# Kernel tuning notes

Measured on AMD Instinct MI355X. Metric: run time of the kernel, lower is better.

Reference implementation:

```python
import jax, jax.numpy as jnp
import numpy as np

D_MODEL, D_STATE, EXPAND = 1024, 128, 2
E = D_MODEL * EXPAND          # 2048
N = D_STATE                   # 128
H = 1
P = E
TD = D_STATE // 2             # 64
Z_DIM = E + E + N + N + H + H + TD + H  # 4369
EPS = 1e-05
B_SZ, L = 4, 2048


def setup_inputs() -> dict:
    key = jax.random.key(0)
    ks = jax.random.split(key, 6)
    u = jax.random.normal(ks[0], (B_SZ, L, D_MODEL), dtype=jnp.float32)
    W_in = jax.random.normal(ks[1], (Z_DIM, D_MODEL), dtype=jnp.float32) * 0.02
    W_out = jax.random.normal(ks[2], (D_MODEL, E), dtype=jnp.float32) * 0.02
    w_normB = jnp.ones((N,), jnp.float32)
    w_normC = jnp.ones((N,), jnp.float32)
    B_bias = jnp.ones((N,), jnp.float32)
    C_bias = jnp.ones((N,), jnp.float32)
    # dt_bias buffer: dt_i ~ logU(0.001, 0.1); dt_bias = dt_i + log(-expm1(-dt_i))
    dt_i = jnp.exp(jax.random.uniform(ks[3], (H,)) * (np.log(0.1) - np.log(0.001)) + np.log(0.001))
    dt_i = jnp.clip(dt_i, 1e-4, None)
    dt_bias = dt_i + jnp.log(-jnp.expm1(-dt_i))
    A_log = jnp.full((H,), np.log(0.5), jnp.float32)
    return {"u": u, "W_in": W_in, "w_normB": w_normB, "w_normC": w_normC,
            "B_bias": B_bias, "C_bias": C_bias, "dt_bias": dt_bias,
            "A_log": A_log, "W_out": W_out}


def _rms(x, w):
    return x * jax.lax.rsqrt(jnp.mean(x * x, axis=-1, keepdims=True) + EPS) * w


def _rope(x, ang):
    half = x.shape[-1] // 2
    x1, x2 = x[..., :half], x[..., half:]
    c, s = jnp.cos(ang), jnp.sin(ang)
    return jnp.concatenate([x1 * c - x2 * s, x1 * s + x2 * c], axis=-1)


def reference(u, W_in, w_normB, w_normC, B_bias, C_bias, dt_bias, A_log, W_out):
    Bb, Ls, _ = u.shape
    z = u @ W_in.T  # [B, L, Z_DIM]
    o = 0
    def take(n):
        nonlocal o
        r = z[..., o:o + n]; o += n; return r
    x = jax.nn.silu(take(E))
    gate = jax.nn.silu(take(E))
    B_ = take(N)
    C_ = take(N)
    dt_ = take(H)
    A_ = take(H)
    th = take(TD)
    lam_ = take(H)

    dt = jax.nn.softplus(dt_ + dt_bias)          # [B, L, H]
    A = -jax.nn.softplus(A_ + A_log)             # [B, L, H]
    lam = jax.nn.sigmoid(lam_)                   # [B, L, H]
    alpha = jnp.exp(dt * A)                      # [B, L, H]

    B_ = _rms(B_, w_normB) + B_bias
    C_ = _rms(C_, w_normC) + C_bias
    ca = jnp.cumsum(jnp.mean(dt, axis=-1, keepdims=True) * th, axis=1)  # [B, L, TD]
    B_ = _rope(B_, ca)
    C_ = _rope(C_, ca)

    xh = x.reshape(Bb, Ls, H, P)
    xp = jnp.concatenate([jnp.zeros_like(xh[:, :1]), xh[:, :-1]], axis=1)  # roll + zero t=0
    lh = lam[..., None]
    xt = lh * xh + (1.0 - lh) * alpha[..., None] * xp  # [B, L, H, P]

    # fallback SSM: per-channel mean drive, per-head scalar A (mean over batch+time)
    u_mean = jnp.mean(xt, axis=-1)               # [B, L, H]
    A_bar = jnp.mean(A, axis=(0, 1))             # [H]
    dA = jnp.exp(dt * A_bar)                     # [B, L, H]
    dBu = dt[..., None] * B_[:, :, None, :] * u_mean[..., None]  # [B, L, H, N]

    def step(state, xs):
        dA_t, dBu_t, C_t = xs                    # [B,H], [B,H,N], [B,N]
        state = dA_t[..., None] * state + dBu_t  # [B, H, N]
        y_t = jnp.einsum('bhn,bn->bh', state, C_t)
        return state, y_t

    state0 = jnp.zeros((Bb, H, N), dtype=xt.dtype)
    _, ys = jax.lax.scan(step, state0,
                         (jnp.moveaxis(dA, 1, 0), jnp.moveaxis(dBu, 1, 0), jnp.moveaxis(C_, 1, 0)))
    outs = jnp.moveaxis(ys, 0, 1)                # [B, L, H]
    y = jnp.broadcast_to(outs, (Bb, Ls, E))      # H=1 expanded to E
    return (y * gate) @ W_out.T
```

## Files before the change

### kernel.cpp

```cpp
#include <hip/hip_runtime.h>
#include <cstdint>
#include <cstddef>

typedef __bf16 bf16_t;
typedef bf16_t bf16x8 __attribute__((ext_vector_type(8)));
typedef float f32x4 __attribute__((ext_vector_type(4)));

#define B_SZ    4
#define LSEQ    2048
#define DMODEL  1024
#define EDIM    2048
#define NSTATE  128
#define ZDIM    4419
#define ZPAD    4608
#define ROWS    (B_SZ*LSEQ)
#define EPSV    1e-5f

#define SCHUNK  128
#define SCLEN   (LSEQ/SCHUNK)
#define RCH     128
#define RCLEN   (LSEQ/RCH)

__device__ __forceinline__ float softplus_f(float x){
  return fmaxf(x, 0.f) + log1pf(expf(-fabsf(x)));
}
__device__ __forceinline__ float sigmoid_f(float x){ return 1.f/(1.f+expf(-x)); }
__device__ __forceinline__ float silu_f(float x){ return x/(1.f+expf(-x)); }

__device__ __forceinline__ void gload_lds16(const void* g, void* l){
  __builtin_amdgcn_global_load_lds(
      (const __attribute__((address_space(1))) void*)g,
      (__attribute__((address_space(3))) void*)l, 16, 0, 0);
}

__device__ __forceinline__ float blockReduce256(float v, float* red, int t){
  red[t] = v; __syncthreads();
  #pragma unroll
  for (int off = 128; off > 0; off >>= 1){
    if (t < off) red[t] += red[t+off];
    __syncthreads();
  }
  float r = red[0];
  __syncthreads();
  return r;
}

__global__ __launch_bounds__(256) void prep_kernel(
    const float* __restrict__ u, const float* __restrict__ win, const float* __restrict__ wout,
    bf16_t* __restrict__ ubf, bf16_t* __restrict__ winbf, bf16_t* __restrict__ woutbf,
    float* __restrict__ Asum)
{
  size_t i = (size_t)blockIdx.x*256 + threadIdx.x;
  if (i == 0) Asum[0] = 0.f;
  const size_t NU = (size_t)ROWS*DMODEL;
  const size_t NW = (size_t)ZPAD*DMODEL;
  const size_t NO = (size_t)DMODEL*EDIM;
  if (i < NU){ ubf[i] = (bf16_t)u[i]; return; }
  i -= NU;
  if (i < NW){
    size_t n = i >> 10;
    winbf[i] = (n < (size_t)ZDIM) ? (bf16_t)win[i] : (bf16_t)0.f;
    return;
  }
  i -= NW;
  if (i < NO) woutbf[i] = (bf16_t)wout[i];
}

template<int BM, int KDIM, int MODE>
__global__ __launch_bounds__(512, 2) void gemm8_kernel(
    const bf16_t* __restrict__ A, const bf16_t* __restrict__ W,
    bf16_t* __restrict__ o_x, bf16_t* __restrict__ o_g, float* __restrict__ o_z,
    const float* __restrict__ scale, float* __restrict__ o_f)
{
  constexpr int BN  = 256;
  constexpr int NT  = KDIM/64;
  constexpr int MR  = BM/32;
  constexpr int BUFE = (BM+BN)*64;
  __shared__ __align__(16) bf16_t lds[BUFE*2];

  const int tid  = threadIdx.x;
  const int wid  = tid>>6, lane = tid&63;
  const int wr   = wid>>2, wc = wid&3;
  const int m0   = blockIdx.y*BM, n0 = blockIdx.x*BN;
  const int lr   = lane&15;

  f32x4 acc[MR][4] = {};

  auto stage = [&](int buf, int t){
    bf16_t* lA = lds + buf*BUFE;
    bf16_t* lB = lA + BM*64;
    const int k0 = t*64;
    #pragma unroll
    for (int q = 0; q < BM/64; ++q){
      int cidx = q*512 + tid;
      int row = cidx>>3, sc = (cidx&7) ^ (row&7);
      gload_lds16(A + (size_t)(m0+row)*KDIM + k0 + sc*8,
                  lA + (size_t)(q*512 + wid*64)*8);
    }
    #pragma unroll
    for (int q = 0; q < BN/64; ++q){
      int cidx = q*512 + tid;
      int row = cidx>>3, sc = (cidx&7) ^ (row&7);
      gload_lds16(W + (size_t)(n0+row)*KDIM + k0 + sc*8,
                  lB + (size_t)(q*512 + wid*64)*8);
    }
  };

  stage(0, 0);
  __syncthreads();
  int cur = 0;
  for (int t = 0; t < NT; ++t){
    if (t+1 < NT) stage(cur^1, t+1);
    const bf16_t* lA = lds + cur*BUFE;
    const bf16_t* lB = lA + BM*64;
    #pragma unroll
    for (int kk = 0; kk < 2; ++kk){
      const int g = kk*4 + (lane>>4);
      bf16x8 bfr[4], af[MR];
      #pragma unroll
      for (int n = 0; n < 4; ++n){
        int rr = wc*64 + n*16 + lr;
        bfr[n] = *(const bf16x8*)&lB[rr*64 + ((g^(rr&7))<<3)];
      }
      #pragma unroll
      for (int m = 0; m < MR; ++m){
        int rr = wr*(BM/2) + m*16 + lr;
        af[m] = *(const bf16x8*)&lA[rr*64 + ((g^(rr&7))<<3)];
      }
      __builtin_amdgcn_s_setprio(1);
      #pragma unroll
      for (int m = 0; m < MR; ++m)
        #pragma unroll
        for (int n = 0; n < 4; ++n)
          acc[m][n] = __builtin_amdgcn_mfma_f32_16x16x32_bf16(af[m], bfr[n], acc[m][n], 0,0,0);
      __builtin_amdgcn_s_setprio(0);
    }
    __syncthreads();
    cur ^= 1;
  }

  #pragma unroll
  for (int m = 0; m < MR; ++m){
    int rowb = m0 + wr*(BM/2) + m*16 + ((lane>>4)<<2);
    #pragma unroll
    for (int n = 0; n < 4; ++n){
      int col = n0 + wc*64 + n*16 + lr;
      #pragma unroll
      for (int i = 0; i < 4; ++i){
        int r = rowb + i;
        float v = acc[m][n][i];
        if (MODE == 0){
          if (col < 2048)       o_x[(size_t)r*EDIM + col]        = (bf16_t)silu_f(v);
          else if (col < 4096)  o_g[(size_t)r*EDIM + (col-2048)] = (bf16_t)silu_f(v);
          else if (col < 4480)  o_z[(size_t)r*384 + (col-4096)]  = v;
        } else {
          o_f[(size_t)r*DMODEL + col] = v * scale[r];
        }
      }
    }
  }
}

__global__ __launch_bounds__(256) void fuse_kernel(
    const bf16_t* __restrict__ xbuf, const float* __restrict__ zs,
    const float* __restrict__ wnB, const float* __restrict__ wnC,
    const float* __restrict__ Bb, const float* __restrict__ Cb,
    const float* __restrict__ dtb, const float* __restrict__ Alog,
    float* __restrict__ Bn, float* __restrict__ Cn, float* __restrict__ dtth,
    float* __restrict__ dts, float* __restrict__ alphas, float* __restrict__ lams,
    float* __restrict__ xbar, float* Asum)
{
  __shared__ float red[256];
  int r = blockIdx.x, t = threadIdx.x;

  const bf16_t* xr = xbuf + (size_t)r*EDIM;
  bf16x8 xv = *(const bf16x8*)(xr + t*8);
  float s = 0.f;
  #pragma unroll
  for (int i=0;i<8;++i) s += (float)xv[i];
  float xs = blockReduce256(s, red, t);

  const float* zr = zs + (size_t)r*384;
  float dt  = softplus_f(zr[256] + dtb[0]);
  float Av  = -softplus_f(zr[257] + Alog[0]);
  float lam = sigmoid_f(zr[322]);
  float alpha = expf(dt*Av);

  if (t == 0){
    xbar[r]   = xs * (1.f/2048.f);
    dts[r]    = dt;
    alphas[r] = alpha;
    lams[r]   = lam;
    atomicAdd(Asum, Av);
  }
  if (t < 64) dtth[(size_t)r*64 + t] = dt * zr[258+t];

  float bv = (t < 128) ? zr[t]       : 0.f;
  float cv = (t < 128) ? zr[128+t]   : 0.f;
  float b2 = blockReduce256(bv*bv, red, t);
  float c2 = blockReduce256(cv*cv, red, t);
  if (t < 128){
    float rb = rsqrtf(b2*(1.f/128.f) + EPSV);
    float rc = rsqrtf(c2*(1.f/128.f) + EPSV);
    Bn[(size_t)r*128 + t] = bv*rb*wnB[t] + Bb[t];
    Cn[(size_t)r*128 + t] = cv*rc*wnC[t] + Cb[t];
  }
}

__global__ __launch_bounds__(64) void rope_sum_kernel(
    const float* __restrict__ dtth, float* __restrict__ csum)
{
  int b  = blockIdx.x >> 7;
  int ch = blockIdx.x & 127;
  int d  = threadIdx.x;
  const float* base = dtth + ((size_t)b*LSEQ + (size_t)ch*RCLEN)*64 + d;
  float s = 0.f;
  #pragma unroll
  for (int i = 0; i < RCLEN; ++i) s += base[(size_t)i*64];
  csum[((size_t)b*RCH + ch)*64 + d] = s;
}

__global__ __launch_bounds__(64) void rope_prefix_kernel(float* __restrict__ csum)
{
  int b = blockIdx.x, d = threadIdx.x;
  float s = 0.f;
  for (int c = 0; c < RCH; ++c){
    size_t idx = ((size_t)b*RCH + c)*64 + d;
    float v = csum[idx]; csum[idx] = s; s += v;
  }
}

__global__ __launch_bounds__(64) void rope_apply_kernel(
    const float* __restrict__ dtth, const float* __restrict__ csum,
    float* __restrict__ Bn, float* __restrict__ Cn)
{
  int b  = blockIdx.x >> 7;
  int ch = blockIdx.x & 127;
  int d  = threadIdx.x;
  float ca = csum[((size_t)b*RCH + ch)*64 + d];
  int l0 = ch*RCLEN;
  const float* base = dtth + ((size_t)b*LSEQ)*64 + d;
  for (int l = l0; l < l0 + RCLEN; ++l){
    ca += base[(size_t)l*64];
    float sn, cs;
    sincosf(ca, &sn, &cs);
    size_t ro = ((size_t)b*LSEQ + l)*128;
    float b1 = Bn[ro+d], b2v = Bn[ro+64+d];
    Bn[ro+d]    = b1*cs - b2v*sn;
    Bn[ro+64+d] = b1*sn + b2v*cs;
    float c1 = Cn[ro+d], c2v = Cn[ro+64+d];
    Cn[ro+d]    = c1*cs - c2v*sn;
    Cn[ro+64+d] = c1*sn + c2v*cs;
  }
}

__global__ __launch_bounds__(64) void scan_local_kernel(
    const float* __restrict__ dts, const float* __restrict__ alphas,
    const float* __restrict__ lams, const float* __restrict__ xbar,
    const float* __restrict__ Asum,
    const float* __restrict__ Bn, const float* __restrict__ Cn,
    float* __restrict__ ylocal, float* __restrict__ Pfix,
    float* __restrict__ Sfin, float* __restrict__ Dch)
{
  int b  = blockIdx.x / SCHUNK;
  int ch = blockIdx.x % SCHUNK;
  int n  = threadIdx.x;
  float Abar = Asum[0] * (1.f/(float)ROWS);
  float s1 = 0.f, s2 = 0.f, P = 1.f;
  int l0 = ch*SCLEN;
  #pragma unroll
  for (int i = 0; i < SCLEN; ++i){
    int l = l0 + i;
    size_t r = (size_t)b*LSEQ + l;
    float dt = dts[r], lam = lams[r], al = alphas[r], xb = xbar[r];
    float xp = (l > 0) ? xbar[r-1] : 0.f;
    float um = lam*xb + (1.f-lam)*al*xp;
    float dA = expf(dt*Abar);
    float coef = dt*um;
    size_t ro = r*128;
    s1 = dA*s1 + coef*Bn[ro+n];
    s2 = dA*s2 + coef*Bn[ro+64+n];
    P *= dA;
    float p = s1*Cn[ro+n] + s2*Cn[ro+64+n];
    #pragma unroll
    for (int off = 32; off > 0; off >>= 1) p += __shfl_down(p, off);
    if (n == 0){ ylocal[r] = p; Pfix[r] = P; }
  }
  size_t so = ((size_t)b*SCHUNK + ch)*128;
  Sfin[so + n]      = s1;
  Sfin[so + 64 + n] = s2;
  if (n == 0) Dch[b*SCHUNK + ch] = P;
}

__global__ __launch_bounds__(128) void scan_carry_kernel(
    const float* __restrict__ Sfin, const float* __restrict__ Dch,
    float* __restrict__ Sin)
{
  int b = blockIdx.x;
  int n = threadIdx.x;
  float s = 0.f;
  for (int c = 0; c < SCHUNK; ++c){
    size_t so = ((size_t)b*SCHUNK + c)*128;
    Sin[so + n] = s;
    s = Dch[b*SCHUNK + c]*s + Sfin[so + n];
  }
}

__global__ __launch_bounds__(256) void scan_fix_kernel(
    const float* __restrict__ Cn, const float* __restrict__ Sin,
    const float* __restrict__ ylocal, const float* __restrict__ Pfix,
    float* __restrict__ outsv)
{
  int r = blockIdx.x*4 + (threadIdx.x>>6);
  int n = threadIdx.x & 63;
  int b  = r / LSEQ;
  int ch = (r % LSEQ) / SCLEN;
  const float* si = Sin + ((size_t)b*SCHUNK + ch)*128;
  size_t ro = (size_t)r*128;
  float p = Cn[ro+n]*si[n] + Cn[ro+64+n]*si[64+n];
  #pragma unroll
  for (int off = 32; off > 0; off >>= 1) p += __shfl_down(p, off);
  if (n == 0) outsv[r] = ylocal[r] + Pfix[r]*p;
}

extern "C" void kernel_launch(void* const* d_in, const int* in_sizes, int n_in,
                              void* d_out, int out_size, void* d_ws, size_t ws_size,
                              hipStream_t stream)
{
  const float* u    = (const float*)d_in[0];
  const float* W_in = (const float*)d_in[1];
  const float* wnB  = (const float*)d_in[2];
  const float* wnC  = (const float*)d_in[3];
  const float* Bb   = (const float*)d_in[4];
  const float* Cb   = (const float*)d_in[5];
  const float* dtb  = (const float*)d_in[6];
  const float* Alog = (const float*)d_in[7];
  const float* Wout = (const float*)d_in[8];
  float* out = (float*)d_out;
  char* ws = (char*)d_ws;

  constexpr size_t OFF_ASUM = 0;
  constexpr size_t OFF_UBF  = 256;
  constexpr size_t SZ_UBF   = (size_t)ROWS*DMODEL*2;
  constexpr size_t OFF_WIN  = OFF_UBF + SZ_UBF;
  constexpr size_t SZ_WIN   = (size_t)ZPAD*DMODEL*2;
  constexpr size_t OFF_WOUT = OFF_WIN + SZ_WIN;
  constexpr size_t SZ_WOUT  = (size_t)DMODEL*EDIM*2;
  constexpr size_t OFF_X    = OFF_WOUT + SZ_WOUT;
  constexpr size_t SZ_X     = (size_t)ROWS*EDIM*2;
  constexpr size_t OFF_G    = OFF_X + SZ_X;
  constexpr size_t OFF_ZS   = OFF_G + SZ_X;
  constexpr size_t SZ_ZS    = (size_t)ROWS*384*4;
  constexpr size_t OFF_BN   = OFF_ZS + SZ_ZS;
  constexpr size_t SZ_BN    = (size_t)ROWS*128*4;
  constexpr size_t OFF_CN   = OFF_BN + SZ_BN;
  constexpr size_t OFF_DTTH = OFF_CN + SZ_BN;
  constexpr size_t SZ_DTTH  = (size_t)ROWS*64*4;
  constexpr size_t OFF_DT   = OFF_DTTH + SZ_DTTH;
  constexpr size_t OFF_AL   = OFF_DT  + (size_t)ROWS*4;
  constexpr size_t OFF_LAM  = OFF_AL  + (size_t)ROWS*4;
  constexpr size_t OFF_XB   = OFF_LAM + (size_t)ROWS*4;
  constexpr size_t OFF_OUTS = OFF_XB  + (size_t)ROWS*4;
  constexpr size_t OFF_YLOC = OFF_OUTS + (size_t)ROWS*4;
  constexpr size_t OFF_PFIX = OFF_YLOC + (size_t)ROWS*4;
  constexpr size_t OFF_SFIN = OFF_PFIX + (size_t)ROWS*4;
  constexpr size_t SZ_SFIN  = (size_t)B_SZ*SCHUNK*128*4;
  constexpr size_t OFF_DCH  = OFF_SFIN + SZ_SFIN;
  constexpr size_t OFF_SIN  = OFF_DCH + (size_t)B_SZ*SCHUNK*4;
  constexpr size_t OFF_CSUM = OFF_SIN + SZ_SFIN;

  float*  Asum   = (float*) (ws + OFF_ASUM);
  bf16_t* ubf    = (bf16_t*)(ws + OFF_UBF);
  bf16_t* winbf  = (bf16_t*)(ws + OFF_WIN);
  bf16_t* woutbf = (bf16_t*)(ws + OFF_WOUT);
  bf16_t* xbuf   = (bf16_t*)(ws + OFF_X);
  bf16_t* gbuf   = (bf16_t*)(ws + OFF_G);
  float*  zsb    = (float*) (ws + OFF_ZS);
  float*  Bn     = (float*) (ws + OFF_BN);
  float*  Cn     = (float*) (ws + OFF_CN);
  float*  dtth   = (float*) (ws + OFF_DTTH);
  float*  dts    = (float*) (ws + OFF_DT);
  float*  alphas = (float*) (ws + OFF_AL);
  float*  lams   = (float*) (ws + OFF_LAM);
  float*  xbar   = (float*) (ws + OFF_XB);
  float*  outsv  = (float*) (ws + OFF_OUTS);
  float*  ylocal = (float*) (ws + OFF_YLOC);
  float*  Pfix   = (float*) (ws + OFF_PFIX);
  float*  Sfin   = (float*) (ws + OFF_SFIN);
  float*  Dch    = (float*) (ws + OFF_DCH);
  float*  Sin    = (float*) (ws + OFF_SIN);
  float*  csum   = (float*) (ws + OFF_CSUM);

  {
    size_t total = (size_t)ROWS*DMODEL + (size_t)ZPAD*DMODEL + (size_t)DMODEL*EDIM;
    int blocks = (int)((total + 255)/256);
    prep_kernel<<<blocks, 256, 0, stream>>>(u, W_in, Wout, ubf, winbf, woutbf, Asum);
  }
  {
    dim3 g(ZPAD/256, ROWS/256);
    gemm8_kernel<256, DMODEL, 0><<<g, 512, 0, stream>>>(
        ubf, winbf, xbuf, gbuf, zsb, nullptr, nullptr);
  }
  fuse_kernel<<<ROWS, 256, 0, stream>>>(xbuf, zsb, wnB, wnC, Bb, Cb, dtb, Alog,
                                        Bn, Cn, dtth, dts, alphas, lams, xbar, Asum);
  rope_sum_kernel<<<B_SZ*RCH, 64, 0, stream>>>(dtth, csum);
  rope_prefix_kernel<<<B_SZ, 64, 0, stream>>>(csum);
  rope_apply_kernel<<<B_SZ*RCH, 64, 0, stream>>>(dtth, csum, Bn, Cn);
  scan_local_kernel<<<B_SZ*SCHUNK, 64, 0, stream>>>(dts, alphas, lams, xbar, Asum,
                                                    Bn, Cn, ylocal, Pfix, Sfin, Dch);
  scan_carry_kernel<<<B_SZ, 128, 0, stream>>>(Sfin, Dch, Sin);
  scan_fix_kernel<<<ROWS/4, 256, 0, stream>>>(Cn, Sin, ylocal, Pfix, outsv);
  {
    dim3 g(DMODEL/256, ROWS/128);
    gemm8_kernel<128, EDIM, 1><<<g, 512, 0, stream>>>(
        gbuf, woutbf, nullptr, nullptr, nullptr, outsv, out);
  }
}
```

Before: 344.5 us.

## Fuse x row-mean into GEMM epilogue and triple-buffer GEMM pipeline

The first GEMM no longer writes the silu(x) activations to memory. It reduces them per row in the epilogue and adds the partial sums to an fp32 buffer with atomics, which removes a large bf16 store and its reload in fuse_kernel. The GEMM moves to a 3-stage LDS pipeline with explicit vmcnt waits and raw barriers, a 1D grid with XCD-aware block remapping, and BM=128 for the first GEMM. fuse_kernel shrinks to 128 threads. The cost is atomic contention, a non-deterministic summation order, and larger LDS use that may reduce occupancy.

```diff
diff --git a/kernel.cpp b/kernel.cpp
--- a/kernel.cpp
+++ b/kernel.cpp
@@ -10,7 +10,6 @@
 #define LSEQ    2048
 #define DMODEL  1024
 #define EDIM    2048
-#define NSTATE  128
 #define ZDIM    4419
 #define ZPAD    4608
 #define ROWS    (B_SZ*LSEQ)
@@ -33,10 +32,10 @@
       (__attribute__((address_space(3))) void*)l, 16, 0, 0);
 }
 
-__device__ __forceinline__ float blockReduce256(float v, float* red, int t){
+__device__ __forceinline__ float blockReduce128(float v, float* red, int t){
   red[t] = v; __syncthreads();
   #pragma unroll
-  for (int off = 128; off > 0; off >>= 1){
+  for (int off = 64; off > 0; off >>= 1){
     if (t < off) red[t] += red[t+off];
     __syncthreads();
   }
@@ -48,10 +47,11 @@
 __global__ __launch_bounds__(256) void prep_kernel(
     const float* __restrict__ u, const float* __restrict__ win, const float* __restrict__ wout,
     bf16_t* __restrict__ ubf, bf16_t* __restrict__ winbf, bf16_t* __restrict__ woutbf,
-    float* __restrict__ Asum)
+    float* __restrict__ Asum, float* __restrict__ xraw)
 {
   size_t i = (size_t)blockIdx.x*256 + threadIdx.x;
   if (i == 0) Asum[0] = 0.f;
+  if (i < ROWS) xraw[i] = 0.f;
   const size_t NU = (size_t)ROWS*DMODEL;
   const size_t NW = (size_t)ZPAD*DMODEL;
   const size_t NO = (size_t)DMODEL*EDIM;
@@ -66,23 +66,28 @@
   if (i < NO) woutbf[i] = (bf16_t)wout[i];
 }
 
-template<int BM, int KDIM, int MODE>
-__global__ __launch_bounds__(512, 2) void gemm8_kernel(
+template<int BM, int KDIM, int NXT, int MODE>
+__global__ __launch_bounds__(512, 2) void gemmDP_kernel(
     const bf16_t* __restrict__ A, const bf16_t* __restrict__ W,
-    bf16_t* __restrict__ o_x, bf16_t* __restrict__ o_g, float* __restrict__ o_z,
+    float* __restrict__ xraw, bf16_t* __restrict__ o_g, float* __restrict__ o_z,
     const float* __restrict__ scale, float* __restrict__ o_f)
 {
-  constexpr int BN  = 256;
-  constexpr int NT  = KDIM/64;
-  constexpr int MR  = BM/32;
+  constexpr int BN = 256;
+  constexpr int NT = KDIM/64;
+  constexpr int MR = BM/32;
   constexpr int BUFE = (BM+BN)*64;
-  __shared__ __align__(16) bf16_t lds[BUFE*2];
-
-  const int tid  = threadIdx.x;
-  const int wid  = tid>>6, lane = tid&63;
-  const int wr   = wid>>2, wc = wid&3;
-  const int m0   = blockIdx.y*BM, n0 = blockIdx.x*BN;
-  const int lr   = lane&15;
+  __shared__ __align__(16) bf16_t lds[BUFE*3];
+
+  const int tid = threadIdx.x;
+  const int wid = tid>>6, lane = tid&63;
+  const int wr = wid>>2, wc = wid&3;
+  const int lr = lane&15;
+
+  const int nwg = NXT*(ROWS/BM);
+  const int id = blockIdx.x;
+  const int rid = (id & 7)*(nwg>>3) + (id>>3);
+  const int bx = rid % NXT, by = rid / NXT;
+  const int m0 = by*BM, n0 = bx*BN;
 
   f32x4 acc[MR][4] = {};
 
@@ -106,12 +111,8 @@
     }
   };
 
-  stage(0, 0);
-  __syncthreads();
-  int cur = 0;
-  for (int t = 0; t < NT; ++t){
-    if (t+1 < NT) stage(cur^1, t+1);
-    const bf16_t* lA = lds + cur*BUFE;
+  auto compute = [&](int buf){
+    const bf16_t* lA = lds + buf*BUFE;
     const bf16_t* lB = lA + BM*64;
     #pragma unroll
     for (int kk = 0; kk < 2; ++kk){
@@ -135,34 +136,70 @@
           acc[m][n] = __builtin_amdgcn_mfma_f32_16x16x32_bf16(af[m], bfr[n], acc[m][n], 0,0,0);
       __builtin_amdgcn_s_setprio(0);
     }
-    __syncthreads();
-    cur ^= 1;
-  }
-
-  #pragma unroll
-  for (int m = 0; m < MR; ++m){
-    int rowb = m0 + wr*(BM/2) + m*16 + ((lane>>4)<<2);
-    #pragma unroll
-    for (int n = 0; n < 4; ++n){
-      int col = n0 + wc*64 + n*16 + lr;
+  };
+
+  stage(0, 0);
+  stage(1, 1);
+  int cur = 0;
+  for (int t = 0; t + 2 < NT; ++t){
+    int nb = cur + 2; if (nb >= 3) nb -= 3;
+    stage(nb, t+2);
+    asm volatile("s_waitcnt vmcnt(12)" ::: "memory");
+    asm volatile("s_barrier" ::: "memory");
+    compute(cur);
+    asm volatile("s_barrier" ::: "memory");
+    if (++cur == 3) cur = 0;
+  }
+  asm volatile("s_waitcnt vmcnt(6)" ::: "memory");
+  asm volatile("s_barrier" ::: "memory");
+  compute(cur);
+  asm volatile("s_barrier" ::: "memory");
+  if (++cur == 3) cur = 0;
+  asm volatile("s_waitcnt vmcnt(0)" ::: "memory");
+  asm volatile("s_barrier" ::: "memory");
+  compute(cur);
+
+  if (MODE == 0 && n0 < 2048){
+    #pragma unroll
+    for (int m = 0; m < MR; ++m){
       #pragma unroll
       for (int i = 0; i < 4; ++i){
-        int r = rowb + i;
-        float v = acc[m][n][i];
-        if (MODE == 0){
-          if (col < 2048)       o_x[(size_t)r*EDIM + col]        = (bf16_t)silu_f(v);
-          else if (col < 4096)  o_g[(size_t)r*EDIM + (col-2048)] = (bf16_t)silu_f(v);
-          else if (col < 4480)  o_z[(size_t)r*384 + (col-4096)]  = v;
-        } else {
-          o_f[(size_t)r*DMODEL + col] = v * scale[r];
+        float p = 0.f;
+        #pragma unroll
+        for (int n = 0; n < 4; ++n) p += silu_f(acc[m][n][i]);
+        #pragma unroll
+        for (int off = 8; off > 0; off >>= 1) p += __shfl_xor(p, off);
+        if (lr == 0){
+          int r = m0 + wr*(BM/2) + m*16 + ((lane>>4)<<2) + i;
+          atomicAdd(xraw + r, p);
         }
       }
     }
-  }
-}
-
-__global__ __launch_bounds__(256) void fuse_kernel(
-    const bf16_t* __restrict__ xbuf, const float* __restrict__ zs,
+  } else {
+    #pragma unroll
+    for (int m = 0; m < MR; ++m){
+      int rowb = m0 + wr*(BM/2) + m*16 + ((lane>>4)<<2);
+      #pragma unroll
+      for (int n = 0; n < 4; ++n){
+        int col = n0 + wc*64 + n*16 + lr;
+        #pragma unroll
+        for (int i = 0; i < 4; ++i){
+          int r = rowb + i;
+          float v = acc[m][n][i];
+          if (MODE == 0){
+            if (col < 4096)      o_g[(size_t)r*EDIM + (col-2048)] = (bf16_t)silu_f(v);
+            else if (col < 4480) o_z[(size_t)r*384 + (col-4096)]  = v;
+          } else {
+            o_f[(size_t)r*DMODEL + col] = v * scale[r];
+          }
+        }
+      }
+    }
+  }
+}
+
+__global__ __launch_bounds__(128) void fuse_kernel(
+    const float* __restrict__ xraw, const float* __restrict__ zs,
     const float* __restrict__ wnB, const float* __restrict__ wnC,
     const float* __restrict__ Bb, const float* __restrict__ Cb,
     const float* __restrict__ dtb, const float* __restrict__ Alog,
@@ -170,40 +207,27 @@
     float* __restrict__ dts, float* __restrict__ alphas, float* __restrict__ lams,
     float* __restrict__ xbar, float* Asum)
 {
-  __shared__ float red[256];
+  __shared__ float red[128];
   int r = blockIdx.x, t = threadIdx.x;
-
-  const bf16_t* xr = xbuf + (size_t)r*EDIM;
-  bf16x8 xv = *(const bf16x8*)(xr + t*8);
-  float s = 0.f;
-  #pragma unroll
-  for (int i=0;i<8;++i) s += (float)xv[i];
-  float xs = blockReduce256(s, red, t);
-
   const float* zr = zs + (size_t)r*384;
-  float dt  = softplus_f(zr[256] + dtb[0]);
-  float Av  = -softplus_f(zr[257] + Alog[0]);
-  float lam = sigmoid_f(zr[322]);
-  float alpha = expf(dt*Av);
-
+  float bv = zr[t], cv = zr[128+t];
+  float b2 = blockReduce128(bv*bv, red, t);
+  float c2 = blockReduce128(cv*cv, red, t);
+  float rb = rsqrtf(b2*(1.f/128.f) + EPSV);
+  float rc = rsqrtf(c2*(1.f/128.f) + EPSV);
+  Bn[(size_t)r*128 + t] = bv*rb*wnB[t] + Bb[t];
+  Cn[(size_t)r*128 + t] = cv*rc*wnC[t] + Cb[t];
+
+  float dt = softplus_f(zr[256] + dtb[0]);
+  if (t < 64) dtth[(size_t)r*64 + t] = dt * zr[258+t];
   if (t == 0){
-    xbar[r]   = xs * (1.f/2048.f);
+    float Av  = -softplus_f(zr[257] + Alog[0]);
+    float lam = sigmoid_f(zr[322]);
     dts[r]    = dt;
-    alphas[r] = alpha;
+    alphas[r] = expf(dt*Av);
     lams[r]   = lam;
+    xbar[r]   = xraw[r] * (1.f/2048.f);
     atomicAdd(Asum, Av);
-  }
-  if (t < 64) dtth[(size_t)r*64 + t] = dt * zr[258+t];
-
-  float bv = (t < 128) ? zr[t]       : 0.f;
-  float cv = (t < 128) ? zr[128+t]   : 0.f;
-  float b2 = blockReduce256(bv*bv, red, t);
-  float c2 = blockReduce256(cv*cv, red, t);
-  if (t < 128){
-    float rb = rsqrtf(b2*(1.f/128.f) + EPSV);
-    float rc = rsqrtf(c2*(1.f/128.f) + EPSV);
-    Bn[(size_t)r*128 + t] = bv*rb*wnB[t] + Bb[t];
-    Cn[(size_t)r*128 + t] = cv*rc*wnC[t] + Cb[t];
   }
 }
 
@@ -373,7 +397,7 @@
   bf16_t* ubf    = (bf16_t*)(ws + OFF_UBF);
   bf16_t* winbf  = (bf16_t*)(ws + OFF_WIN);
   bf16_t* woutbf = (bf16_t*)(ws + OFF_WOUT);
-  bf16_t* xbuf   = (bf16_t*)(ws + OFF_X);
+  float*  xraw   = (float*) (ws + OFF_X);
   bf16_t* gbuf   = (bf16_t*)(ws + OFF_G);
   float*  zsb    = (float*) (ws + OFF_ZS);
   float*  Bn     = (float*) (ws + OFF_BN);
@@ -394,14 +418,11 @@
   {
     size_t total = (size_t)ROWS*DMODEL + (size_t)ZPAD*DMODEL + (size_t)DMODEL*EDIM;
     int blocks = (int)((total + 255)/256);
-    prep_kernel<<<blocks, 256, 0, stream>>>(u, W_in, Wout, ubf, winbf, woutbf, Asum);
-  }
-  {
-    dim3 g(ZPAD/256, ROWS/256);
-    gemm8_kernel<256, DMODEL, 0><<<g, 512, 0, stream>>>(
-        ubf, winbf, xbuf, gbuf, zsb, nullptr, nullptr);
-  }
-  fuse_kernel<<<ROWS, 256, 0, stream>>>(xbuf, zsb, wnB, wnC, Bb, Cb, dtb, Alog,
+    prep_kernel<<<blocks, 256, 0, stream>>>(u, W_in, Wout, ubf, winbf, woutbf, Asum, xraw);
+  }
+  gemmDP_kernel<128, DMODEL, ZPAD/256, 0><<<(ZPAD/256)*(ROWS/128), 512, 0, stream>>>(
+      ubf, winbf, xraw, gbuf, zsb, nullptr, nullptr);
+  fuse_kernel<<<ROWS, 128, 0, stream>>>(xraw, zsb, wnB, wnC, Bb, Cb, dtb, Alog,
                                         Bn, Cn, dtth, dts, alphas, lams, xbar, Asum);
   rope_sum_kernel<<<B_SZ*RCH, 64, 0, stream>>>(dtth, csum);
   rope_prefix_kernel<<<B_SZ, 64, 0, stream>>>(csum);
@@ -410,9 +431,6 @@
                                                     Bn, Cn, ylocal, Pfix, Sfin, Dch);
   scan_carry_kernel<<<B_SZ, 128, 0, stream>>>(Sfin, Dch, Sin);
   scan_fix_kernel<<<ROWS/4, 256, 0, stream>>>(Cn, Sin, ylocal, Pfix, outsv);
-  {
-    dim3 g(DMODEL/256, ROWS/128);
-    gemm8_kernel<128, EDIM, 1><<<g, 512, 0, stream>>>(
-        gbuf, woutbf, nullptr, nullptr, nullptr, outsv, out);
-  }
-}
+  gemmDP_kernel<128, EDIM, DMODEL/256, 1><<<(DMODEL/256)*(ROWS/128), 512, 0, stream>>>(
+      gbuf, woutbf, nullptr, nullptr, nullptr, outsv, out);
+}
```

Measured after the change: 338.0 us. No clear change (-1.9%).
